# Optimization experiments

Hardware: AMD Instinct MI355X
Metric: run time of the kernel (lower is better)

Reference implementation:

```python
import jax, jax.numpy as jnp
import numpy as np

B, D, Q = 64, 1024, 128
V, E, H = 50000, 300, 256   # vocab, embed_dim, prealign hidden
POS_V, POS_D = 56, 12
NER_V, NER_D = 19, 8


def setup_inputs() -> dict:
    key = jax.random.key(0)
    ks = jax.random.split(key, 10)
    word_emb = (jax.random.normal(ks[0], (V, E), jnp.float32) * 0.1).at[0].set(0.0)
    pos_emb = (jax.random.normal(ks[1], (POS_V, POS_D), jnp.float32) * 0.1).at[0].set(0.0)
    ner_emb = (jax.random.normal(ks[2], (NER_V, NER_D), jnp.float32) * 0.1).at[0].set(0.0)
    proj_w = jax.random.normal(ks[3], (E, H), jnp.float32) / np.sqrt(E)
    proj_b = jnp.zeros((H,), jnp.float32)
    return {
        "query_tok": jax.random.randint(ks[4], (B, Q), 0, V),
        "doc_tok": jax.random.randint(ks[5], (B, D), 0, V),
        "doc_pos": jax.random.randint(ks[6], (B, D), 0, POS_V),
        "doc_ner": jax.random.randint(ks[7], (B, D), 0, NER_V),
        "doc_fea": jax.random.normal(ks[8], (B, D, 4), jnp.float32),
        "word_emb": word_emb,
        "proj_w": proj_w,
        "proj_b": proj_b,
        "pos_emb": pos_emb,
        "ner_emb": ner_emb,
    }


def _embed(table, idx):
    # padding_idx=0 semantics: row 0 contributes zeros
    return table[idx] * (idx != 0)[..., None].astype(table.dtype)


def reference(query_tok, doc_tok, doc_pos, doc_ner, doc_fea,
              word_emb, proj_w, proj_b, pos_emb, ner_emb):
    doc_e = _embed(word_emb, doc_tok)      # [B,D,E]
    query_e = _embed(word_emb, query_tok)  # [B,Q,E]

    # Prealign: shared Linear+ReLU proj, then bmm -> softmax -> bmm
    d_proj = jax.nn.relu(doc_e @ proj_w + proj_b)    # [B,D,H]
    q_proj = jax.nn.relu(query_e @ proj_w + proj_b)  # [B,Q,H]
    scores = jnp.einsum('bdh,bqh->bdq', d_proj, q_proj)
    attn = jax.nn.softmax(scores, axis=-1)           # softmax over query dim
    prealign = jnp.einsum('bdq,bqe->bde', attn, query_e)  # [B,D,E]

    doc_out = jnp.concatenate(
        [doc_e, prealign, _embed(ner_emb, doc_ner), _embed(pos_emb, doc_pos), doc_fea],
        axis=-1)  # [B,D,E+E+8+12+4]
    return query_e, doc_out
```

## Files before the change

kernel.cpp:

```cpp
#include <hip/hip_runtime.h>
#include <hip/hip_bf16.h>

typedef unsigned short u16;
typedef __attribute__((ext_vector_type(8))) short bf16x8;
typedef __attribute__((ext_vector_type(4))) float f32x4;

#define MFMA16(a, b, c) __builtin_amdgcn_mfma_f32_16x16x32_bf16((a), (b), (c), 0, 0, 0)

#define NB 64
#define ND 1024
#define NQ 128
#define NE 300
#define NH 256
#define KP 320
#define QETN 304
#define DOC_W 624

static __device__ __forceinline__ u16 f2bf(float f) {
  union { __bf16 h; u16 u; } c; c.h = (__bf16)f; return c.u;
}

static __device__ __forceinline__ bf16x8 pack8(float4 f0, float4 f1) {
  union { bf16x8 v; u16 u[8]; } r;
  r.u[0] = f2bf(f0.x); r.u[1] = f2bf(f0.y); r.u[2] = f2bf(f0.z); r.u[3] = f2bf(f0.w);
  r.u[4] = f2bf(f1.x); r.u[5] = f2bf(f1.y); r.u[6] = f2bf(f1.z); r.u[7] = f2bf(f1.w);
  return r.v;
}

static __device__ __forceinline__ bf16x8 cvt8(const float* p) {
  return pack8(*(const float4*)p, *(const float4*)(p + 4));
}

__global__ void k_aux(const float* __restrict__ w, u16* __restrict__ wt,
                      const int* __restrict__ qtok, const float* __restrict__ table,
                      float* __restrict__ q_out,
                      const int* __restrict__ ner, const int* __restrict__ pos,
                      const float* __restrict__ fea,
                      const float* __restrict__ ner_emb, const float* __restrict__ pos_emb,
                      float* __restrict__ doc_out) {
  int bx = blockIdx.x;
  if (bx < 320) {
    int idx = bx * 256 + threadIdx.x;
    int n = idx / KP, k = idx % KP;
    wt[idx] = (k < NE) ? f2bf(w[k * NH + n]) : (u16)0;
  } else if (bx < 2720) {
    int idx = (bx - 320) * 256 + threadIdx.x;
    int row = idx / 75, j = idx % 75;
    int k = j * 4;
    float4 v = {0.f, 0.f, 0.f, 0.f};
    int t = qtok[row];
    if (t != 0) v = *(const float4*)(table + (long)t * NE + k);
    *(float4*)(q_out + (long)row * NE + k) = v;
  } else {
    int idx = (bx - 2720) * 256 + threadIdx.x;
    int row = idx / 6, c0 = (idx % 6) * 4;
    float4 v;
    float* vp = (float*)&v;
#pragma unroll
    for (int u = 0; u < 4; ++u) {
      int c = c0 + u;
      float x;
      if (c < 8)       { int t = ner[row]; x = t ? ner_emb[t * 8 + c] : 0.f; }
      else if (c < 20) { int t = pos[row]; x = t ? pos_emb[t * 12 + (c - 8)] : 0.f; }
      else             { x = fea[(long)row * 4 + (c - 20)]; }
      vp[u] = x;
    }
    *(float4*)(doc_out + (long)row * DOC_W + 600 + c0) = v;
  }
}

__launch_bounds__(256)
__global__ void k_qside(const float* __restrict__ qo, const u16* __restrict__ Wt,
                        const float* __restrict__ bias,
                        u16* __restrict__ qP, u16* __restrict__ qet) {
  __shared__ u16 T[64][314];
  int tid = threadIdx.x;
  if (blockIdx.x < 128) {
    int l = tid & 63, w = tid >> 6;
    int lr = l & 15, lg = l >> 4;
    int bm = blockIdx.x * 64 + (w & 1) * 32;
    int bn = (w >> 1) * 128;
    f32x4 acc[2][8] = {};
    const float* xp0 = qo + (long)(bm + lr) * NE + 8 * lg;
    const float* xp1 = xp0 + 16 * NE;
    const u16* wp = Wt + (long)(bn + lr) * KP + 8 * lg;
#pragma unroll 2
    for (int ks = 0; ks < KP; ks += 32) {
      bf16x8 a0 = cvt8(xp0 + ks);
      bf16x8 a1 = cvt8(xp1 + ks);
#pragma unroll
      for (int nt = 0; nt < 8; ++nt) {
        bf16x8 b0 = *(const bf16x8*)(wp + (long)nt * 16 * KP + ks);
        acc[0][nt] = MFMA16(a0, b0, acc[0][nt]);
        acc[1][nt] = MFMA16(a1, b0, acc[1][nt]);
      }
    }
#pragma unroll
    for (int nt = 0; nt < 8; ++nt) {
      int col = bn + nt * 16 + lr;
      float bv = bias[col];
#pragma unroll
      for (int mt = 0; mt < 2; ++mt)
#pragma unroll
        for (int r = 0; r < 4; ++r) {
          int row = bm + mt * 16 + 4 * lg + r;
          float v = acc[mt][nt][r] + bv;
          v = v > 0.f ? v : 0.f;
          qP[(long)row * NH + col] = f2bf(v);
        }
    }
  } else {
    int bx = blockIdx.x - 128;
    int b = bx >> 1, k0 = (bx & 1) * 64;
    const float* src = qo + ((long)b * NQ + k0) * NE;
    for (int i = tid; i < 64 * 75; i += 256) {
      int row = i / 75, j = (i % 75) * 4;
      float4 f = *(const float4*)(src + (long)row * NE + j);
      T[row][j]     = f2bf(f.x); T[row][j + 1] = f2bf(f.y);
      T[row][j + 2] = f2bf(f.z); T[row][j + 3] = f2bf(f.w);
    }
    __syncthreads();
    u16* dst = qet + (long)b * QETN * NQ + k0;
    for (int i = tid; i < QETN * 16; i += 256) {
      int n = i / 16, kq = (i % 16) * 4;
      u16 v[4] = {0, 0, 0, 0};
      if (n < NE) {
        v[0] = T[kq][n]; v[1] = T[kq + 1][n]; v[2] = T[kq + 2][n]; v[3] = T[kq + 3][n];
      }
      *(uint2*)(dst + (long)n * NQ + kq) = *(const uint2*)v;
    }
  }
}

__launch_bounds__(256, 2)
__global__ void k_fused(const int* __restrict__ dtok, const float* __restrict__ emb,
                        float* doc_out, const u16* __restrict__ Wt,
                        const float* __restrict__ bias,
                        const u16* __restrict__ qP, const u16* __restrict__ qeT) {
  __shared__ __align__(16) u16 dp[128][264];
  u16 (*p_lds)[136] = (u16 (*)[136]) & dp[0][0];
  int b = blockIdx.y, chunk = blockIdx.x;
  int l = threadIdx.x & 63, w = threadIdx.x >> 6;
  int lr = l & 15, lg = l >> 4;
  long blkrow = (long)b * ND + chunk * 128;

  {
    int mrow0 = (w & 1) * 64;
    int ncol0 = (w >> 1) * 128;
    bool wr = (w >> 1) == 0;
    const float* arow[4];
    float* drow[4];
#pragma unroll
    for (int mt = 0; mt < 4; ++mt) {
      long r = blkrow + mrow0 + mt * 16 + lr;
      arow[mt] = emb + (long)dtok[r] * NE;
      drow[mt] = doc_out + r * DOC_W;
    }
    const u16* wp = Wt + (long)(ncol0 + lr) * KP + 8 * lg;
    f32x4 acc[4][8] = {};
    int c0 = 8 * lg;
#pragma unroll 3
    for (int ks = 0; ks < 288; ks += 32) {
      bf16x8 a[4];
#pragma unroll
      for (int mt = 0; mt < 4; ++mt) {
        int col = ks + c0;
        float4 f0 = *(const float4*)(arow[mt] + col);
        float4 f1 = *(const float4*)(arow[mt] + col + 4);
        if (wr) {
          *(float4*)(drow[mt] + col) = f0;
          *(float4*)(drow[mt] + col + 4) = f1;
        }
        a[mt] = pack8(f0, f1);
      }
      __builtin_amdgcn_s_setprio(1);
#pragma unroll
      for (int nt = 0; nt < 8; ++nt) {
        bf16x8 bb = *(const bf16x8*)(wp + nt * 16 * KP + ks);
#pragma unroll
        for (int mt = 0; mt < 4; ++mt) acc[mt][nt] = MFMA16(a[mt], bb, acc[mt][nt]);
      }
      __builtin_amdgcn_s_setprio(0);
    }
    {
      const int ks = 288;
      int col = ks + c0;
      float4 z = {0.f, 0.f, 0.f, 0.f};
      bf16x8 a[4];
#pragma unroll
      for (int mt = 0; mt < 4; ++mt) {
        float4 f0 = (col + 4 <= NE) ? *(const float4*)(arow[mt] + col) : z;
        float4 f1 = (col + 8 <= NE) ? *(const float4*)(arow[mt] + col + 4) : z;
        if (wr) {
          if (col + 4 <= NE) *(float4*)(drow[mt] + col) = f0;
          if (col + 8 <= NE) *(float4*)(drow[mt] + col + 4) = f1;
        }
        a[mt] = pack8(f0, f1);
      }
      __builtin_amdgcn_s_setprio(1);
#pragma unroll
      for (int nt = 0; nt < 8; ++nt) {
        bf16x8 bb = *(const bf16x8*)(wp + nt * 16 * KP + ks);
#pragma unroll
        for (int mt = 0; mt < 4; ++mt) acc[mt][nt] = MFMA16(a[mt], bb, acc[mt][nt]);
      }
      __builtin_amdgcn_s_setprio(0);
    }
#pragma unroll
    for (int nt = 0; nt < 8; ++nt) {
      int col = ncol0 + nt * 16 + lr;
      float bv = bias[col];
#pragma unroll
      for (int mt = 0; mt < 4; ++mt)
#pragma unroll
        for (int r = 0; r < 4; ++r) {
          float v = acc[mt][nt][r] + bv;
          dp[mrow0 + mt * 16 + 4 * lg + r][col] = f2bf(v > 0.f ? v : 0.f);
        }
    }
  }

  const u16* qpp = qP + ((long)b * NQ + lr) * NH + 8 * lg;
  bf16x8 qb[8];
#pragma unroll
  for (int nt = 0; nt < 8; ++nt) qb[nt] = *(const bf16x8*)(qpp + (long)nt * 16 * NH);
  __syncthreads();

  f32x4 s[2][8] = {};
  {
    {
      bf16x8 a0 = *(const bf16x8*)&dp[w * 32 + lr][8 * lg];
      bf16x8 a1 = *(const bf16x8*)&dp[w * 32 + 16 + lr][8 * lg];
      __builtin_amdgcn_s_setprio(1);
#pragma unroll
      for (int nt = 0; nt < 8; ++nt) {
        s[0][nt] = MFMA16(a0, qb[nt], s[0][nt]);
        s[1][nt] = MFMA16(a1, qb[nt], s[1][nt]);
      }
      __builtin_amdgcn_s_setprio(0);
    }
#pragma unroll
    for (int ks = 32; ks < NH; ks += 32) {
      bf16x8 a0 = *(const bf16x8*)&dp[w * 32 + lr][ks + 8 * lg];
      bf16x8 a1 = *(const bf16x8*)&dp[w * 32 + 16 + lr][ks + 8 * lg];
      __builtin_amdgcn_s_setprio(1);
#pragma unroll
      for (int nt = 0; nt < 8; ++nt) {
        bf16x8 bb = *(const bf16x8*)(qpp + (long)nt * 16 * NH + ks);
        s[0][nt] = MFMA16(a0, bb, s[0][nt]);
        s[1][nt] = MFMA16(a1, bb, s[1][nt]);
      }
      __builtin_amdgcn_s_setprio(0);
    }
  }
  __syncthreads();

#pragma unroll
  for (int mt = 0; mt < 2; ++mt) {
    f32x4 mx;
#pragma unroll
    for (int r = 0; r < 4; ++r) {
      float m = s[mt][0][r];
#pragma unroll
      for (int nt = 1; nt < 8; ++nt) m = fmaxf(m, s[mt][nt][r]);
      mx[r] = m;
    }
#pragma unroll
    for (int d = 1; d < 16; d <<= 1)
#pragma unroll
      for (int r = 0; r < 4; ++r) mx[r] = fmaxf(mx[r], __shfl_xor(mx[r], d));
    f32x4 sum = {};
#pragma unroll
    for (int nt = 0; nt < 8; ++nt)
#pragma unroll
      for (int r = 0; r < 4; ++r) {
        float p = __expf(s[mt][nt][r] - mx[r]);
        s[mt][nt][r] = p;
        sum[r] += p;
      }
#pragma unroll
    for (int d = 1; d < 16; d <<= 1)
#pragma unroll
      for (int r = 0; r < 4; ++r) sum[r] += __shfl_xor(sum[r], d);
    f32x4 inv;
#pragma unroll
    for (int r = 0; r < 4; ++r) inv[r] = 1.0f / sum[r];
#pragma unroll
    for (int nt = 0; nt < 8; ++nt)
#pragma unroll
      for (int r = 0; r < 4; ++r)
        p_lds[w * 32 + mt * 16 + 4 * lg + r][nt * 16 + lr] = f2bf(s[mt][nt][r] * inv[r]);
  }

  const u16* qtp = qeT + (long)b * QETN * NQ;
  bf16x8 pa[2][4];
#pragma unroll
  for (int mt = 0; mt < 2; ++mt)
#pragma unroll
    for (int ksi = 0; ksi < 4; ++ksi)
      pa[mt][ksi] = *(const bf16x8*)&p_lds[w * 32 + mt * 16 + lr][ksi * 32 + 8 * lg];
#pragma unroll 2
  for (int nt = 0; nt < 19; ++nt) {
    f32x4 acc0 = {}, acc1 = {};
    __builtin_amdgcn_s_setprio(1);
#pragma unroll
    for (int ksi = 0; ksi < 4; ++ksi) {
      bf16x8 bb = *(const bf16x8*)(qtp + (long)(nt * 16 + lr) * NQ + ksi * 32 + 8 * lg);
      acc0 = MFMA16(pa[0][ksi], bb, acc0);
      acc1 = MFMA16(pa[1][ksi], bb, acc1);
    }
    __builtin_amdgcn_s_setprio(0);
    int col = nt * 16 + lr;
    if (col < NE) {
#pragma unroll
      for (int r = 0; r < 4; ++r) {
        long rl0 = blkrow + w * 32 + 4 * lg + r;
        doc_out[rl0 * DOC_W + 300 + col] = acc0[r];
        doc_out[(rl0 + 16) * DOC_W + 300 + col] = acc1[r];
      }
    }
  }
}

extern "C" void kernel_launch(void* const* d_in, const int* in_sizes, int n_in,
                              void* d_out, int out_size, void* d_ws, size_t ws_size,
                              hipStream_t stream) {
  const int *query_tok = nullptr, *doc_tok = nullptr, *doc_pos = nullptr, *doc_ner = nullptr;
  const float *doc_fea = nullptr, *word_emb = nullptr, *proj_w = nullptr,
              *proj_b = nullptr, *pos_emb = nullptr, *ner_emb = nullptr;
  int n65536 = 0;
  for (int i = 0; i < n_in; ++i) {
    switch (in_sizes[i]) {
      case 15000000: word_emb  = (const float*)d_in[i]; break;
      case 262144:   doc_fea   = (const float*)d_in[i]; break;
      case 76800:    proj_w    = (const float*)d_in[i]; break;
      case 8192:     query_tok = (const int*)d_in[i];   break;
      case 256:      proj_b    = (const float*)d_in[i]; break;
      case 672:      pos_emb   = (const float*)d_in[i]; break;
      case 152:      ner_emb   = (const float*)d_in[i]; break;
      case 65536:
        if (n65536 == 0)      doc_tok = (const int*)d_in[i];
        else if (n65536 == 1) doc_pos = (const int*)d_in[i];
        else                  doc_ner = (const int*)d_in[i];
        ++n65536; break;
      default: break;
    }
  }

  float* out = (float*)d_out;
  float* q_out   = out;
  float* doc_out = out + (size_t)NB * NQ * NE;

  char* ws = (char*)d_ws;
  u16* Wt  = (u16*)ws; ws += (size_t)NH * KP * 2;
  u16* qP  = (u16*)ws; ws += (size_t)NB * NQ * NH * 2;
  u16* qeT = (u16*)ws; ws += (size_t)NB * QETN * NQ * 2;

  k_aux<<<dim3(4256), dim3(256), 0, stream>>>(
      proj_w, Wt, query_tok, word_emb, q_out,
      doc_ner, doc_pos, doc_fea, ner_emb, pos_emb, doc_out);
  k_qside<<<dim3(256), dim3(256), 0, stream>>>(q_out, Wt, proj_b, qP, qeT);
  k_fused<<<dim3(ND / 128, NB), dim3(256), 0, stream>>>(
      doc_tok, word_emb, doc_out, Wt, proj_b, qP, qeT);
}
```

Before: 131.1 us.

## Split doc projection into two N-halves with triple-buffered embedding prefetch

The doc projection GEMM is now done in two passes over 64-column halves of the hidden dimension, which halves the accumulator registers per pass. Each pass runs a fully unrolled K loop with a three-deep register buffer that prefetches gathered embedding rows two steps ahead, so global load latency overlaps with MFMA work. The cost is that each embedding row is gathered twice, once per half; only the first pass writes the doc_e copy. The buffers add register pressure, which the smaller accumulator footprint is meant to offset.

```diff
diff --git a/kernel.cpp b/kernel.cpp
--- a/kernel.cpp
+++ b/kernel.cpp
@@ -143,11 +143,11 @@
   int l = threadIdx.x & 63, w = threadIdx.x >> 6;
   int lr = l & 15, lg = l >> 4;
   long blkrow = (long)b * ND + chunk * 128;
+  int c0 = 8 * lg;
 
   {
     int mrow0 = (w & 1) * 64;
     int ncol0 = (w >> 1) * 128;
-    bool wr = (w >> 1) == 0;
     const float* arow[4];
     float* drow[4];
 #pragma unroll
@@ -156,67 +156,81 @@
       arow[mt] = emb + (long)dtok[r] * NE;
       drow[mt] = doc_out + r * DOC_W;
     }
-    const u16* wp = Wt + (long)(ncol0 + lr) * KP + 8 * lg;
-    f32x4 acc[4][8] = {};
-    int c0 = 8 * lg;
-#pragma unroll 3
-    for (int ks = 0; ks < 288; ks += 32) {
-      bf16x8 a[4];
-#pragma unroll
-      for (int mt = 0; mt < 4; ++mt) {
-        int col = ks + c0;
-        float4 f0 = *(const float4*)(arow[mt] + col);
-        float4 f1 = *(const float4*)(arow[mt] + col + 4);
+    const float4 z4 = {0.f, 0.f, 0.f, 0.f};
+#pragma unroll 1
+    for (int h = 0; h < 2; ++h) {
+      const u16* wp = Wt + (long)(ncol0 + h * 64 + lr) * KP + c0;
+      bool wr = (h == 0) && ((w >> 1) == 0);
+      f32x4 acc[4][4] = {};
+      float4 buf[3][8];
+#pragma unroll
+      for (int j = 0; j < 2; ++j)
+#pragma unroll
+        for (int mt = 0; mt < 4; ++mt) {
+          int col = j * 32 + c0;
+          buf[j][2 * mt]     = *(const float4*)(arow[mt] + col);
+          buf[j][2 * mt + 1] = *(const float4*)(arow[mt] + col + 4);
+        }
+#pragma unroll
+      for (int i = 0; i < 10; ++i) {
+        if (i < 8) {
+          int j = i + 2, s = j % 3;
+          int col = j * 32 + c0;
+          if (j < 9) {
+#pragma unroll
+            for (int mt = 0; mt < 4; ++mt) {
+              buf[s][2 * mt]     = *(const float4*)(arow[mt] + col);
+              buf[s][2 * mt + 1] = *(const float4*)(arow[mt] + col + 4);
+            }
+          } else {
+#pragma unroll
+            for (int mt = 0; mt < 4; ++mt) {
+              buf[s][2 * mt]     = (col + 4 <= NE) ? *(const float4*)(arow[mt] + col) : z4;
+              buf[s][2 * mt + 1] = (col + 8 <= NE) ? *(const float4*)(arow[mt] + col + 4) : z4;
+            }
+          }
+        }
+        int s = i % 3;
+        int col = i * 32 + c0;
         if (wr) {
-          *(float4*)(drow[mt] + col) = f0;
-          *(float4*)(drow[mt] + col + 4) = f1;
-        }
-        a[mt] = pack8(f0, f1);
-      }
-      __builtin_amdgcn_s_setprio(1);
-#pragma unroll
-      for (int nt = 0; nt < 8; ++nt) {
-        bf16x8 bb = *(const bf16x8*)(wp + nt * 16 * KP + ks);
-#pragma unroll
-        for (int mt = 0; mt < 4; ++mt) acc[mt][nt] = MFMA16(a[mt], bb, acc[mt][nt]);
-      }
-      __builtin_amdgcn_s_setprio(0);
-    }
-    {
-      const int ks = 288;
-      int col = ks + c0;
-      float4 z = {0.f, 0.f, 0.f, 0.f};
-      bf16x8 a[4];
-#pragma unroll
-      for (int mt = 0; mt < 4; ++mt) {
-        float4 f0 = (col + 4 <= NE) ? *(const float4*)(arow[mt] + col) : z;
-        float4 f1 = (col + 8 <= NE) ? *(const float4*)(arow[mt] + col + 4) : z;
-        if (wr) {
-          if (col + 4 <= NE) *(float4*)(drow[mt] + col) = f0;
-          if (col + 8 <= NE) *(float4*)(drow[mt] + col + 4) = f1;
-        }
-        a[mt] = pack8(f0, f1);
-      }
-      __builtin_amdgcn_s_setprio(1);
-#pragma unroll
-      for (int nt = 0; nt < 8; ++nt) {
-        bf16x8 bb = *(const bf16x8*)(wp + nt * 16 * KP + ks);
-#pragma unroll
-        for (int mt = 0; mt < 4; ++mt) acc[mt][nt] = MFMA16(a[mt], bb, acc[mt][nt]);
-      }
-      __builtin_amdgcn_s_setprio(0);
-    }
-#pragma unroll
-    for (int nt = 0; nt < 8; ++nt) {
-      int col = ncol0 + nt * 16 + lr;
-      float bv = bias[col];
-#pragma unroll
-      for (int mt = 0; mt < 4; ++mt)
-#pragma unroll
-        for (int r = 0; r < 4; ++r) {
-          float v = acc[mt][nt][r] + bv;
-          dp[mrow0 + mt * 16 + 4 * lg + r][col] = f2bf(v > 0.f ? v : 0.f);
-        }
+          if (i < 9) {
+#pragma unroll
+            for (int mt = 0; mt < 4; ++mt) {
+              *(float4*)(drow[mt] + col) = buf[s][2 * mt];
+              *(float4*)(drow[mt] + col + 4) = buf[s][2 * mt + 1];
+            }
+          } else {
+#pragma unroll
+            for (int mt = 0; mt < 4; ++mt) {
+              if (col + 4 <= NE) *(float4*)(drow[mt] + col) = buf[s][2 * mt];
+              if (col + 8 <= NE) *(float4*)(drow[mt] + col + 4) = buf[s][2 * mt + 1];
+            }
+          }
+        }
+        bf16x8 a[4];
+#pragma unroll
+        for (int mt = 0; mt < 4; ++mt) a[mt] = pack8(buf[s][2 * mt], buf[s][2 * mt + 1]);
+        __builtin_amdgcn_s_setprio(1);
+#pragma unroll
+        for (int nt = 0; nt < 4; ++nt) {
+          bf16x8 bb = *(const bf16x8*)(wp + nt * 16 * KP + i * 32);
+#pragma unroll
+          for (int mt = 0; mt < 4; ++mt) acc[mt][nt] = MFMA16(a[mt], bb, acc[mt][nt]);
+        }
+        __builtin_amdgcn_s_setprio(0);
+      }
+#pragma unroll
+      for (int nt = 0; nt < 4; ++nt) {
+        int col = ncol0 + h * 64 + nt * 16 + lr;
+        float bv = bias[col];
+#pragma unroll
+        for (int mt = 0; mt < 4; ++mt)
+#pragma unroll
+          for (int r = 0; r < 4; ++r) {
+            float v = acc[mt][nt][r] + bv;
+            dp[mrow0 + mt * 16 + 4 * lg + r][col] = f2bf(v > 0.f ? v : 0.f);
+          }
+      }
     }
   }
 
```

Result: slower. 325.4 us (+148.1%).
